# Performance work log

Hardware: AMD Instinct MI355X
Metric: run time of the kernel (lower is better)

## Reference

```python
import jax, jax.numpy as jnp
import numpy as np

B, T, N, R, I = 32, 512, 1024, 4, 8
DT = 0.1
G = 0.9


def setup_inputs() -> dict:
    key = jax.random.key(0)
    k1, k2, k3, k4, k5 = jax.random.split(key, 5)
    inputs = jax.random.normal(k1, (B, T, I, 1), dtype=jnp.float32)
    f = jax.random.normal(k2, (B, T, R, 1), dtype=jnp.float32)
    J = jax.random.normal(k3, (B, N, N), dtype=jnp.float32) * (G / np.sqrt(N))
    wIn = jax.random.normal(k4, (B, N, I), dtype=jnp.float32)
    m = jax.random.normal(k5, (B, N, R), dtype=jnp.float32)
    return {"inputs": inputs, "f": f, "J": J, "wIn": wIn, "m": m}


def _run(inputs, f, J, wIn, m):
    dt = DT
    dtype = inputs.dtype
    x0 = jnp.zeros((B, N, 1), dtype)
    n0 = jnp.zeros((B, N, R), dtype)
    P0 = jnp.tile(jnp.eye(N, dtype=dtype)[None] / 10.0, (B, 1, 1))

    def step(carry, t_in):
        x, P, n = carry
        u, f_t = t_in                               # u: (B,I,1), f_t: (B,R,1)
        # recurrence (r, z computed from PRE-update x, matching original)
        r = jnp.tanh(x)                             # (B,N,1)
        z = jnp.einsum('bnk,bns->bks', n, r)        # n^T @ r -> (B,R,1)
        x_new = (1.0 - dt) * x + dt * (J @ r + m @ z + wIn @ u)
        # RLS update (uses r from pre-update x)
        Pr = P @ r                                  # (B,N,1)
        rPr = jnp.sum(r * Pr, axis=1, keepdims=True)  # r^T P r -> (B,1,1)
        c = 1.0 / (1.0 + rPr)                       # scalar per batch
        P_new = P - c * (Pr @ jnp.swapaxes(Pr, -1, -2))
        err = z - f_t                               # (B,R,1)
        n_new = n - c * (Pr @ jnp.swapaxes(err, -1, -2))
        return (x_new, P_new, n_new), (x_new, z)

    u_seq = jnp.swapaxes(inputs, 0, 1)              # (T,B,I,1)
    f_seq = jnp.swapaxes(f, 0, 1)                   # (T,B,R,1)
    _, (xs, zs) = jax.lax.scan(step, (x0, P0, n0), (u_seq, f_seq))
    all_x = jnp.swapaxes(xs, 0, 1)                  # (B,T,N,1)
    all_z = jnp.swapaxes(zs, 0, 1)                  # (B,T,R,1)
    return all_x, all_z


def reference(inputs, f, J, wIn, m):
    return _run(inputs, f, J, wIn, m)
```

## Files before the change

### kernel.cpp

```cpp
#include <hip/hip_runtime.h>
#include <hip/hip_bf16.h>

#define BB 32
#define TT 512
#define NN 1024
#define RR 4
#define II 8
#define DT_C 0.1f

#define BPB 32
#define GRID (BB * BPB)

#define NBLK 32
#define ROWS (NN / NBLK)
#define VBLK 16

typedef __attribute__((ext_vector_type(8))) unsigned short ushort8v;

__device__ __forceinline__ float bf2f(unsigned short u) {
    union { unsigned int ui; float f; } cv; cv.ui = ((unsigned int)u) << 16; return cv.f;
}
__device__ __forceinline__ float bf2f_lo(unsigned int u) {
    union { unsigned int ui; float f; } cv; cv.ui = u << 16; return cv.f;
}
__device__ __forceinline__ float bf2f_hi(unsigned int u) {
    union { unsigned int ui; float f; } cv; cv.ui = u & 0xffff0000u; return cv.f;
}
__device__ __forceinline__ unsigned short f2bf_rne(float x) {
    union { float f; unsigned int ui; } cv; cv.f = x;
    unsigned int u = cv.ui; u += 0x7FFFu + ((u >> 16) & 1u);
    return (unsigned short)(u >> 16);
}
__device__ __forceinline__ float wave_reduce(float v) {
    #pragma unroll
    for (int off = 32; off; off >>= 1) v += __shfl_down(v, off, 64);
    return v;
}

__device__ __forceinline__ float llc_ldf(const float* p) {
    float r;
    asm volatile("global_load_dword %0, %1, off sc0 sc1\n\ts_waitcnt vmcnt(0)"
                 : "=&v"(r) : "v"(p) : "memory");
    return r;
}
__device__ __forceinline__ void llc_stf(float* p, float v) {
    asm volatile("global_store_dword %0, %1, off sc0 sc1" :: "v"(p), "v"(v) : "memory");
}
__device__ __forceinline__ void llc_st8(float* p, float a, float b) {
    float2 v; v.x = a; v.y = b;
    asm volatile("global_store_dwordx2 %0, %1, off sc0 sc1" :: "v"(p), "v"(v) : "memory");
}

__global__ __launch_bounds__(256) void k_convJl(const float* __restrict__ J,
                                                unsigned int* __restrict__ Jl) {
    const int b = blockIdx.x >> 5, k = blockIdx.x & 31;
    const int w = threadIdx.x >> 6, l = threadIdx.x & 63;
    unsigned int* dst = Jl + ((((size_t)(b * 32 + k) * 4 + w) * 64 + l) * 64);
    #pragma unroll
    for (int j = 0; j < 8; ++j) {
        const int row = k * 32 + w * 8 + j;
        const float* __restrict__ Jrow = J + ((size_t)b * NN + row) * NN;
        unsigned int out[8];
        #pragma unroll
        for (int e2 = 0; e2 < 8; ++e2) {
            const int c0 = l + 128 * e2;
            out[e2] = (unsigned int)f2bf_rne(Jrow[c0]) |
                      ((unsigned int)f2bf_rne(Jrow[c0 + 64]) << 16);
        }
        *(uint4*)(dst + j * 8)     = make_uint4(out[0], out[1], out[2], out[3]);
        *(uint4*)(dst + j * 8 + 4) = make_uint4(out[4], out[5], out[6], out[7]);
    }
}

__device__ __forceinline__ void batch_barrier(unsigned* cnt, unsigned* gen,
                                              unsigned expect) {
    asm volatile("s_waitcnt vmcnt(0) lgkmcnt(0)" ::: "memory");
    __syncthreads();
    if (threadIdx.x == 0) {
        unsigned old = __hip_atomic_fetch_add(cnt, 1u, __ATOMIC_RELAXED,
                                              __HIP_MEMORY_SCOPE_AGENT);
        if (old == BPB - 1u) {
            __hip_atomic_store(cnt, 0u, __ATOMIC_RELAXED, __HIP_MEMORY_SCOPE_AGENT);
            asm volatile("s_waitcnt vmcnt(0)" ::: "memory");
            __hip_atomic_fetch_add(gen, 1u, __ATOMIC_RELAXED, __HIP_MEMORY_SCOPE_AGENT);
        } else {
            while (__hip_atomic_load(gen, __ATOMIC_RELAXED, __HIP_MEMORY_SCOPE_AGENT)
                   < expect)
                __builtin_amdgcn_s_sleep(8);
        }
    }
    __syncthreads();
}

__global__ __launch_bounds__(256, 4) void k_persist(
    const unsigned int* __restrict__ Jl,
    float* __restrict__ rbuf,
    float* __restrict__ abuf,
    float* __restrict__ pa,
    float* __restrict__ sqpart,
    float* __restrict__ zr,
    unsigned* __restrict__ cnt, unsigned* __restrict__ gen,
    const float* __restrict__ m, const float* __restrict__ wIn,
    const float* __restrict__ inputs, const float* __restrict__ f,
    float* __restrict__ outx, float* __restrict__ outz)
{
    const int bid = blockIdx.x;
    const int b = (bid & 7) * 4 + (bid >> 8);
    const int k = (bid >> 3) & 31;
    const int tid = threadIdx.x, lane = tid & 63, wave = tid >> 6;
    const int row_loc = tid >> 3, sub = tid & 7;
    const int i_loc = k * 32 + row_loc;

    __shared__ unsigned short V_lds[32][512];
    __shared__ float r_sh[NN];
    __shared__ float a_sh[2 * TT / 2 + 512];
    __shared__ float sq32[32];
    __shared__ float r_next[32];
    __shared__ float Jr_sh[32];
    __shared__ float zred[32][4];
    __shared__ float zr2[128];
    __shared__ float red_sg[4];
    __shared__ float fsh[RR], ush[II], csh[2], zsh[RR], esh[RR];

    unsigned* mycnt = cnt + b * 32;
    unsigned* mygen = gen + b * 32;
    unsigned bar = 0;

    unsigned int jreg[64];
    {
        const uint4* jp = (const uint4*)(Jl +
            ((((size_t)(b * 32 + k) * 4 + wave) * 64 + lane) * 64));
        #pragma unroll
        for (int q = 0; q < 16; ++q) {
            uint4 v = jp[q];
            jreg[q * 4] = v.x; jreg[q * 4 + 1] = v.y;
            jreg[q * 4 + 2] = v.z; jreg[q * 4 + 3] = v.w;
        }
    }
    {
        unsigned long long* vz = (unsigned long long*)&V_lds[0][0];
        for (int q = tid; q < 32 * 512 / 4; q += 256) vz[q] = 0ull;
    }
    float4 nrow = {0.f, 0.f, 0.f, 0.f};
    float xreg = 0.f;
    if (sub == 0) llc_stf(rbuf + b * NN + i_loc, 0.f);
    if (tid < 4)  llc_stf(zr + b * 128 + k * 4 + tid, 0.f);
    batch_barrier(mycnt, mygen, ++bar);

    for (int t = 0; t < TT; ++t) {
        float4 rqf; float2 paw; float zrw;
        {
            const float* rp  = rbuf + b * NN + tid * 4;
            const float* pap = pa + ((size_t)b * 32 + (tid >> 3)) * TT
                                  + k * 16 + (tid & 7) * 2;
            const float* zp  = zr + b * 128 + (tid & 127);
            asm volatile(
                "global_load_dwordx4 %0, %3, off sc0 sc1\n\t"
                "global_load_dwordx2 %1, %4, off sc0 sc1\n\t"
                "global_load_dword   %2, %5, off sc0 sc1\n\t"
                "s_waitcnt vmcnt(0)"
                : "=&v"(rqf), "=&v"(paw), "=&v"(zrw)
                : "v"(rp), "v"(pap), "v"(zp)
                : "memory");
        }
        *(float4*)&r_sh[tid * 4] = rqf;
        zr2[tid & 127] = zrw;
        {
            const int s0g = k * 16 + (tid & 7) * 2;
            a_sh[tid]       = (s0g     < t) ? paw.x : 0.f;
            a_sh[256 + tid] = (s0g + 1 < t) ? paw.y : 0.f;
        }
        if (tid >= 136 && tid < 140) fsh[tid - 136] = f[((size_t)b * TT + t) * RR + (tid - 136)];
        if (tid >= 144 && tid < 152) ush[tid - 144] = inputs[((size_t)b * TT + t) * II + (tid - 144)];
        __syncthreads();
        if (tid < 8) {
            float A = 0.f, B = 0.f;
            #pragma unroll
            for (int kk = 0; kk < 32; ++kk) {
                A += a_sh[kk * 8 + tid];
                B += a_sh[256 + kk * 8 + tid];
            }
            llc_st8(abuf + b * TT + k * 16 + 2 * tid, A, B);
            float sq = A * A + B * B;
            sq += __shfl_down(sq, 4, 8);
            sq += __shfl_down(sq, 2, 8);
            sq += __shfl_down(sq, 1, 8);
            if (tid == 0) llc_stf(sqpart + b * 32 + k, sq);
        }
        batch_barrier(mycnt, mygen, ++bar);

        {
            float2 apw;
            const float* ap = abuf + b * TT + tid * 2;
            asm volatile("global_load_dwordx2 %0, %1, off sc0 sc1\n\ts_waitcnt vmcnt(0)"
                         : "=&v"(apw) : "v"(ap) : "memory");
            a_sh[2 * tid]     = apw.x;
            a_sh[2 * tid + 1] = apw.y;
        }
        {
            float sqr = 0.1f * (rqf.x * rqf.x + rqf.y * rqf.y +
                                rqf.z * rqf.z + rqf.w * rqf.w);
            sqr = wave_reduce(sqr);
            if (lane == 0) red_sg[wave] = sqr;
        }
        if (wave == 0 && lane < 32) sq32[lane] = llc_ldf(sqpart + b * 32 + lane);
        __syncthreads();

        float accJ[8] = {0.f, 0.f, 0.f, 0.f, 0.f, 0.f, 0.f, 0.f};
        #pragma unroll
        for (int e2 = 0; e2 < 8; ++e2) {
            const float rv0 = r_sh[lane + 128 * e2];
            const float rv1 = r_sh[lane + 128 * e2 + 64];
            #pragma unroll
            for (int j = 0; j < 8; ++j) {
                const unsigned int w = jreg[j * 8 + e2];
                accJ[j] = fmaf(bf2f_lo(w), rv0, accJ[j]);
                accJ[j] = fmaf(bf2f_hi(w), rv1, accJ[j]);
            }
        }
        #pragma unroll
        for (int j = 0; j < 8; ++j) {
            float v = wave_reduce(accJ[j]);
            if (lane == 0) Jr_sh[wave * 8 + j] = v;
        }

        if (tid == 0) {
            float sg = red_sg[0] + red_sg[1] + red_sg[2] + red_sg[3];
            float sa = 0.f;
            #pragma unroll
            for (int q = 0; q < 32; ++q) sa += sq32[q];
            const float c = 1.f / (1.f + (sg - sa));
            csh[0] = c; csh[1] = sqrtf(c);
        }
        if (tid < 4) {
            float zq = 0.f;
            #pragma unroll
            for (int kk = 0; kk < 32; ++kk) zq += zr2[kk * 4 + tid];
            zsh[tid] = zq;
            esh[tid] = zq - fsh[tid];
        }
        __syncthreads();

        float accp = 0.f;
        for (int mm = 0; mm * 64 < t; ++mm) {
            const int s0 = mm * 64 + sub * 8;
            const ushort8v vv = *(const ushort8v*)&V_lds[row_loc][s0];
            const float4 a0 = *(const float4*)&a_sh[s0];
            const float4 a1 = *(const float4*)&a_sh[s0 + 4];
            accp = fmaf(bf2f(vv[0]), a0.x, accp);
            accp = fmaf(bf2f(vv[1]), a0.y, accp);
            accp = fmaf(bf2f(vv[2]), a0.z, accp);
            accp = fmaf(bf2f(vv[3]), a0.w, accp);
            accp = fmaf(bf2f(vv[4]), a1.x, accp);
            accp = fmaf(bf2f(vv[5]), a1.y, accp);
            accp = fmaf(bf2f(vv[6]), a1.z, accp);
            accp = fmaf(bf2f(vv[7]), a1.w, accp);
        }
        accp += __shfl_down(accp, 4, 8);
        accp += __shfl_down(accp, 2, 8);
        accp += __shfl_down(accp, 1, 8);

        if (sub == 0) {
            const float c = csh[0], sqc = csh[1];
            const float pr = 0.1f * r_sh[i_loc] - accp;
            V_lds[row_loc][t] = f2bf_rne(sqc * pr);

            float accx = Jr_sh[row_loc];
            const float4 mv = *(const float4*)(m + ((size_t)b * NN + i_loc) * RR);
            accx = fmaf(mv.x, zsh[0], accx); accx = fmaf(mv.y, zsh[1], accx);
            accx = fmaf(mv.z, zsh[2], accx); accx = fmaf(mv.w, zsh[3], accx);
            const float4* __restrict__ wp =
                (const float4*)(wIn + ((size_t)b * NN + i_loc) * II);
            const float4 w0 = wp[0], w1 = wp[1];
            accx = fmaf(w0.x, ush[0], accx); accx = fmaf(w0.y, ush[1], accx);
            accx = fmaf(w0.z, ush[2], accx); accx = fmaf(w0.w, ush[3], accx);
            accx = fmaf(w1.x, ush[4], accx); accx = fmaf(w1.y, ush[5], accx);
            accx = fmaf(w1.z, ush[6], accx); accx = fmaf(w1.w, ush[7], accx);
            const float xn = (1.0f - DT_C) * xreg + DT_C * accx;
            xreg = xn;
            outx[((size_t)b * TT + t) * NN + i_loc] = xn;

            const float cpr = c * pr;
            nrow.x = fmaf(-cpr, esh[0], nrow.x);
            nrow.y = fmaf(-cpr, esh[1], nrow.y);
            nrow.z = fmaf(-cpr, esh[2], nrow.z);
            nrow.w = fmaf(-cpr, esh[3], nrow.w);

            const float rp2 = tanhf(xn);
            r_next[row_loc] = rp2;
            llc_stf(rbuf + b * NN + i_loc, rp2);
            ((float4*)zred)[row_loc] = make_float4(nrow.x * rp2, nrow.y * rp2,
                                                   nrow.z * rp2, nrow.w * rp2);
        }
        __syncthreads();

        if (t < TT - 1 && 2 * tid <= t) {
            const int s0 = 2 * tid;
            float A0 = 0.f, A1 = 0.f;
            #pragma unroll 8
            for (int i = 0; i < 32; ++i) {
                const unsigned vv = *(const unsigned*)&V_lds[i][s0];
                const float rv = r_next[i];
                A0 = fmaf(bf2f_lo(vv), rv, A0);
                A1 = fmaf(bf2f_hi(vv), rv, A1);
            }
            llc_st8(pa + ((size_t)b * 32 + k) * TT + s0, A0, A1);
        }
        if (tid < 4) {
            float zp = 0.f;
            #pragma unroll
            for (int i = 0; i < 32; ++i) zp += zred[i][tid];
            llc_stf(zr + b * 128 + k * 4 + tid, zp);
            if (k == 0) outz[((size_t)b * TT + t) * RR + tid] = zsh[tid];
        }
        batch_barrier(mycnt, mygen, ++bar);
    }
}

__global__ __launch_bounds__(256) void k_convJ_old(const float* __restrict__ J,
                                                   unsigned short* __restrict__ Jp) {
    const int row = blockIdx.x;
    const int tid = threadIdx.x;
    __shared__ float rowsh[NN];
    const float4* __restrict__ src = (const float4*)(J + (size_t)row * NN);
    float4* dst4 = (float4*)rowsh;
    for (int k = tid; k < NN / 4; k += 256) dst4[k] = src[k];
    __syncthreads();
    const int o0 = tid * 4;
    unsigned short out[4];
    #pragma unroll
    for (int j = 0; j < 4; ++j) {
        const int o = o0 + j;
        const int l = (o >> 3) & 63, g = o >> 9, e = o & 7;
        out[j] = f2bf_rne(rowsh[l + 64 * (8 * g + e)]);
    }
    uint2 w;
    w.x = (unsigned int)out[0] | ((unsigned int)out[1] << 16);
    w.y = (unsigned int)out[2] | ((unsigned int)out[3] << 16);
    *(uint2*)(Jp + (size_t)row * NN + o0) = w;
}

__global__ __launch_bounds__(256) void kA_fb(
    const float* __restrict__ x, const unsigned short* __restrict__ Jp,
    const unsigned short* __restrict__ Vp, const float* __restrict__ nmat,
    float* __restrict__ r_out, float* __restrict__ a_out,
    float* __restrict__ Jr, float* __restrict__ zbuf,
    float* __restrict__ part, int t)
{
    const int b   = blockIdx.x / (NBLK + VBLK);
    const int blk = blockIdx.x % (NBLK + VBLK);
    const int tid = threadIdx.x, lane = tid & 63, wave = tid >> 6;

    __shared__ float r_sh[NN];
    __shared__ float red_sh[4];

    for (int j = tid; j < NN; j += 256) {
        const float rv = tanhf(x[b * NN + j]);
        r_sh[j] = rv;
        if (blk == 0) r_out[b * NN + j] = rv;
    }
    __syncthreads();

    if (blk < NBLK) {
        for (int rr = wave; rr < ROWS; rr += 4) {
            const int row = blk * ROWS + rr;
            const ushort8v* __restrict__ Jrow =
                (const ushort8v*)(Jp + ((size_t)b * NN + row) * NN);
            const ushort8v jv0 = Jrow[lane];
            const ushort8v jv1 = Jrow[64 + lane];
            float acc = 0.0f;
            #pragma unroll
            for (int e = 0; e < 8; ++e) acc = fmaf(bf2f(jv0[e]), r_sh[lane + 64 * e], acc);
            #pragma unroll
            for (int e = 0; e < 8; ++e) acc = fmaf(bf2f(jv1[e]), r_sh[lane + 512 + 64 * e], acc);
            acc = wave_reduce(acc);
            if (lane == 0) Jr[b * NN + row] = acc;
        }
        if (blk == 0) {
            float p = 0.0f;
            for (int j = tid; j < NN; j += 256) p = fmaf(r_sh[j], r_sh[j], p);
            p = wave_reduce(p);
            if (lane == 0) red_sh[wave] = p;
            __syncthreads();
            if (tid == 0)
                part[b * 72 + 64] = 0.1f * (red_sh[0] + red_sh[1] + red_sh[2] + red_sh[3]);
            if (wave < RR) {
                float acc = 0.0f;
                for (int i2 = lane; i2 < NN; i2 += 64)
                    acc = fmaf(nmat[((size_t)b * NN + i2) * RR + wave], r_sh[i2], acc);
                acc = wave_reduce(acc);
                if (lane == 0) zbuf[b * RR + wave] = acc;
            }
        }
    } else {
        const int wid = (blk - NBLK) * 4 + wave;
        float negsum = 0.0f;
        for (int s = wid; s < t; s += 64) {
            const ushort8v* __restrict__ col =
                (const ushort8v*)(Vp + ((size_t)b * TT + s) * NN);
            const ushort8v vv0 = col[lane];
            const ushort8v vv1 = col[64 + lane];
            float acc = 0.0f;
            #pragma unroll
            for (int e = 0; e < 8; ++e) acc = fmaf(bf2f(vv0[e]), r_sh[lane + 64 * e], acc);
            #pragma unroll
            for (int e = 0; e < 8; ++e) acc = fmaf(bf2f(vv1[e]), r_sh[lane + 512 + 64 * e], acc);
            acc = wave_reduce(acc);
            if (lane == 0) {
                a_out[b * TT + s] = acc;
                negsum = fmaf(-acc, acc, negsum);
            }
        }
        if (lane == 0) part[b * 72 + wid] = negsum;
    }
}

__global__ __launch_bounds__(256) void kB_fb(
    unsigned short* __restrict__ Vp, const float* __restrict__ r,
    const float* __restrict__ a, const float* __restrict__ Jr,
    const float* __restrict__ zbuf, const float* __restrict__ part,
    float* __restrict__ x, float* __restrict__ nmat,
    const float* __restrict__ m, const float* __restrict__ wIn,
    const float* __restrict__ inputs, const float* __restrict__ f,
    float* __restrict__ outx, float* __restrict__ outz, int t)
{
    const int b   = blockIdx.x >> 3;
    const int tb  = blockIdx.x & 7;
    const int tid = threadIdx.x;
    const int pl    = tid & 63;
    const int slice = tid >> 6;

    __shared__ float a_sh[TT];
    __shared__ float ps[4][128];
    __shared__ float zsh[RR], esh[RR], ush[II];

    for (int s = tid; s < t; s += 256) a_sh[s] = a[b * TT + s];
    if (tid < RR) {
        const float zv = zbuf[b * RR + tid];
        zsh[tid] = zv;
        esh[tid] = zv - f[((size_t)b * TT + t) * RR + tid];
    }
    if (tid >= 64 && tid < 64 + II)
        ush[tid - 64] = inputs[((size_t)b * TT + t) * II + (tid - 64)];
    __syncthreads();

    const int p0 = (tb * 64 + pl) * 2;
    const unsigned short* __restrict__ Vb = Vp + (size_t)b * TT * NN;

    const int s_begin = (t * slice) >> 2;
    const int s_end   = (t * (slice + 1)) >> 2;
    float acc0 = 0.0f, acc1 = 0.0f;
    #pragma unroll 4
    for (int s = s_begin; s < s_end; ++s) {
        const unsigned int w = *(const unsigned int*)(Vb + (size_t)s * NN + p0);
        const float av = a_sh[s];
        acc0 = fmaf(bf2f((unsigned short)(w & 0xFFFFu)), av, acc0);
        acc1 = fmaf(bf2f((unsigned short)(w >> 16)), av, acc1);
    }
    ps[slice][pl * 2]     = acc0;
    ps[slice][pl * 2 + 1] = acc1;
    __syncthreads();

    if (slice == 0) {
        const int l = (p0 >> 3) & 63, g = p0 >> 9, e = p0 & 7;
        const int i0 = l + 64 * (8 * g + e);
        const int i1 = i0 + 64;
        const float s0 = ps[0][pl * 2] + ps[1][pl * 2] + ps[2][pl * 2] + ps[3][pl * 2];
        const float s1 = ps[0][pl * 2 + 1] + ps[1][pl * 2 + 1] + ps[2][pl * 2 + 1] + ps[3][pl * 2 + 1];

        float sg = 0.0f;
        #pragma unroll
        for (int q = 0; q < 65; ++q) sg += part[b * 72 + q];
        const float c  = 1.0f / (1.0f + sg);
        const float sq = sqrtf(c);

        const float pr0 = 0.1f * r[b * NN + i0] - s0;
        const float pr1 = 0.1f * r[b * NN + i1] - s1;

        unsigned int wv = (unsigned int)f2bf_rne(sq * pr0) |
                          ((unsigned int)f2bf_rne(sq * pr1) << 16);
        *(unsigned int*)(Vp + ((size_t)b * TT + t) * NN + p0) = wv;

        #pragma unroll
        for (int which = 0; which < 2; ++which) {
            const int   i  = which ? i1 : i0;
            const float pr = which ? pr1 : pr0;
            float acc = Jr[b * NN + i];
            const float4 mv = *(const float4*)(m + ((size_t)b * NN + i) * RR);
            acc = fmaf(mv.x, zsh[0], acc); acc = fmaf(mv.y, zsh[1], acc);
            acc = fmaf(mv.z, zsh[2], acc); acc = fmaf(mv.w, zsh[3], acc);
            const float4* __restrict__ wp = (const float4*)(wIn + ((size_t)b * NN + i) * II);
            const float4 w0 = wp[0], w1 = wp[1];
            acc = fmaf(w0.x, ush[0], acc); acc = fmaf(w0.y, ush[1], acc);
            acc = fmaf(w0.z, ush[2], acc); acc = fmaf(w0.w, ush[3], acc);
            acc = fmaf(w1.x, ush[4], acc); acc = fmaf(w1.y, ush[5], acc);
            acc = fmaf(w1.z, ush[6], acc); acc = fmaf(w1.w, ush[7], acc);
            const float xo = x[b * NN + i];
            const float xn = (1.0f - DT_C) * xo + DT_C * acc;
            x[b * NN + i] = xn;
            outx[((size_t)b * TT + t) * NN + i] = xn;

            float4* __restrict__ np = (float4*)(nmat + ((size_t)b * NN + i) * RR);
            float4 nv = *np;
            const float cpr = c * pr;
            nv.x = fmaf(-cpr, esh[0], nv.x); nv.y = fmaf(-cpr, esh[1], nv.y);
            nv.z = fmaf(-cpr, esh[2], nv.z); nv.w = fmaf(-cpr, esh[3], nv.w);
            *np = nv;
        }
    }
    if (tb == 0 && tid < RR) outz[((size_t)b * TT + t) * RR + tid] = zsh[tid];
}

extern "C" void kernel_launch(void* const* d_in, const int* in_sizes, int n_in,
                              void* d_out, int out_size, void* d_ws, size_t ws_size,
                              hipStream_t stream) {
    const float* inputs = (const float*)d_in[0];
    const float* f      = (const float*)d_in[1];
    const float* J      = (const float*)d_in[2];
    const float* wIn    = (const float*)d_in[3];
    const float* m      = (const float*)d_in[4];

    float* outx = (float*)d_out;
    float* outz = outx + (size_t)BB * TT * NN;

    char* ws = (char*)d_ws;
    size_t off = 0;
    unsigned int* Jl = (unsigned int*)(ws + off);  off += (size_t)BB * NN * NN * 2;
    unsigned short* Jp_fb = (unsigned short*)Jl;
    unsigned short* V1_fb = (unsigned short*)(ws + off); off += (size_t)BB * TT * NN * 2;
    float* pa     = (float*)(ws + off); off += (size_t)BB * 32 * TT * 4;
    float* rbuf   = (float*)(ws + off); off += (size_t)BB * NN * 4;
    float* abuf   = (float*)(ws + off); off += (size_t)BB * TT * 4;
    float* sqpart = (float*)(ws + off); off += (size_t)BB * 32 * 4;
    float* zrp    = (float*)(ws + off); off += (size_t)BB * 128 * 4;
    unsigned* cnt = (unsigned*)(ws + off); off += (size_t)BB * 32 * 4;
    unsigned* gen = (unsigned*)(ws + off); off += (size_t)BB * 32 * 4;
    float* x_fb   = (float*)(ws + off); off += (size_t)BB * NN * 4;
    float* nm     = (float*)(ws + off); off += (size_t)BB * NN * RR * 4;
    float* Jrb    = (float*)(ws + off); off += (size_t)BB * NN * 4;
    float* zb     = (float*)(ws + off); off += (size_t)BB * RR * 4 + 256;
    float* part72 = (float*)(ws + off); off += (size_t)BB * 72 * 4;

    hipMemsetAsync(cnt, 0, (size_t)BB * 32 * sizeof(unsigned), stream);
    hipMemsetAsync(gen, 0, (size_t)BB * 32 * sizeof(unsigned), stream);
    hipMemsetAsync(x_fb, 0, (size_t)BB * NN * sizeof(float), stream);
    hipMemsetAsync(nm,  0, (size_t)BB * NN * RR * sizeof(float), stream);

    k_convJl<<<BB * 32, 256, 0, stream>>>(J, Jl);

    void* kargs[] = {
        (void*)&Jl, (void*)&rbuf, (void*)&abuf, (void*)&pa,
        (void*)&sqpart, (void*)&zrp,
        (void*)&cnt, (void*)&gen,
        (void*)&m, (void*)&wIn, (void*)&inputs, (void*)&f,
        (void*)&outx, (void*)&outz
    };
    hipError_t rc = hipLaunchCooperativeKernel((const void*)k_persist,
                                               dim3(GRID), dim3(256),
                                               kargs, 0, stream);
    if (rc != hipSuccess) {
        k_convJ_old<<<BB * NN, 256, 0, stream>>>(J, Jp_fb);
        for (int t = 0; t < TT; ++t) {
            kA_fb<<<BB * (NBLK + VBLK), 256, 0, stream>>>(x_fb, Jp_fb, V1_fb, nm,
                                                          rbuf, abuf, Jrb, zb, part72, t);
            kB_fb<<<BB * 8, 256, 0, stream>>>(V1_fb, rbuf, abuf, Jrb, zb, part72,
                                              x_fb, nm, m, wIn, inputs, f, outx, outz, t);
        }
    }
}
```

Before: 9.476 ms.

## Replace per-block partial buffers with atomic accumulation to drop one grid barrier per step

Each step now accumulates the a-vector and z partials directly with device-scope float atomics into a triple-buffered global slot, instead of writing per-block partials, barrier-syncing, and reducing them. This removes one batch-wide barrier and a round of global loads per timestep, and folds the a·a term into the local reduction for c. The V_lds row pitch is padded to 516 to reduce LDS bank conflicts, and the loads are adjusted to fit the new alignment. In exchange it adds atomic contention and makes the summation order nondeterministic. It also needs the future slot to be zeroed ahead of use.

```diff
diff --git a/kernel.cpp b/kernel.cpp
--- a/kernel.cpp
+++ b/kernel.cpp
@@ -15,6 +15,8 @@
 #define ROWS (NN / NBLK)
 #define VBLK 16
 
+#define VPITCH 516
+
 typedef __attribute__((ext_vector_type(8))) unsigned short ushort8v;
 
 __device__ __forceinline__ float bf2f(unsigned short u) {
@@ -37,12 +39,6 @@
     return v;
 }
 
-__device__ __forceinline__ float llc_ldf(const float* p) {
-    float r;
-    asm volatile("global_load_dword %0, %1, off sc0 sc1\n\ts_waitcnt vmcnt(0)"
-                 : "=&v"(r) : "v"(p) : "memory");
-    return r;
-}
 __device__ __forceinline__ void llc_stf(float* p, float v) {
     asm volatile("global_store_dword %0, %1, off sc0 sc1" :: "v"(p), "v"(v) : "memory");
 }
@@ -95,10 +91,8 @@
 __global__ __launch_bounds__(256, 4) void k_persist(
     const unsigned int* __restrict__ Jl,
     float* __restrict__ rbuf,
-    float* __restrict__ abuf,
-    float* __restrict__ pa,
-    float* __restrict__ sqpart,
-    float* __restrict__ zr,
+    float* __restrict__ aalt,
+    float* __restrict__ zslot,
     unsigned* __restrict__ cnt, unsigned* __restrict__ gen,
     const float* __restrict__ m, const float* __restrict__ wIn,
     const float* __restrict__ inputs, const float* __restrict__ f,
@@ -111,14 +105,12 @@
     const int row_loc = tid >> 3, sub = tid & 7;
     const int i_loc = k * 32 + row_loc;
 
-    __shared__ unsigned short V_lds[32][512];
+    __shared__ unsigned short V_lds[32][VPITCH];
     __shared__ float r_sh[NN];
-    __shared__ float a_sh[2 * TT / 2 + 512];
-    __shared__ float sq32[32];
+    __shared__ float a_sh[TT];
+    __shared__ float zred[32][4];
     __shared__ float r_next[32];
     __shared__ float Jr_sh[32];
-    __shared__ float zred[32][4];
-    __shared__ float zr2[128];
     __shared__ float red_sg[4];
     __shared__ float fsh[RR], ush[II], csh[2], zsh[RR], esh[RR];
 
@@ -138,73 +130,67 @@
         }
     }
     {
-        unsigned long long* vz = (unsigned long long*)&V_lds[0][0];
-        for (int q = tid; q < 32 * 512 / 4; q += 256) vz[q] = 0ull;
+        unsigned int* vz = (unsigned int*)&V_lds[0][0];
+        for (int q = tid; q < 32 * VPITCH / 2; q += 256) vz[q] = 0u;
     }
     float4 nrow = {0.f, 0.f, 0.f, 0.f};
     float xreg = 0.f;
     if (sub == 0) llc_stf(rbuf + b * NN + i_loc, 0.f);
-    if (tid < 4)  llc_stf(zr + b * 128 + k * 4 + tid, 0.f);
+    if (tid < 8) {
+        llc_st8(aalt + ((size_t)b * 3 + 0) * 512 + k * 16 + 2 * tid, 0.f, 0.f);
+        llc_st8(aalt + ((size_t)b * 3 + 1) * 512 + k * 16 + 2 * tid, 0.f, 0.f);
+    }
+    if (k == 0 && tid < 16) llc_stf(zslot + b * 24 + tid, 0.f);
     batch_barrier(mycnt, mygen, ++bar);
 
+    int cur = 0;
     for (int t = 0; t < TT; ++t) {
-        float4 rqf; float2 paw; float zrw;
+        const int nxt = (cur == 2) ? 0 : cur + 1;
+        const int fut = (nxt == 2) ? 0 : nxt + 1;
+        float* acur = aalt + ((size_t)b * 3 + cur) * 512;
+        float* anxt = aalt + ((size_t)b * 3 + nxt) * 512;
+        float* afut = aalt + ((size_t)b * 3 + fut) * 512;
+        float* zcur = zslot + (b * 3 + cur) * 8;
+        float* znxt = zslot + (b * 3 + nxt) * 8;
+        float* zfut = zslot + (b * 3 + fut) * 8;
+
+        float4 rqf; float2 aw; float zw;
         {
-            const float* rp  = rbuf + b * NN + tid * 4;
-            const float* pap = pa + ((size_t)b * 32 + (tid >> 3)) * TT
-                                  + k * 16 + (tid & 7) * 2;
-            const float* zp  = zr + b * 128 + (tid & 127);
+            const float* rp = rbuf + b * NN + tid * 4;
+            const float* ap = acur + tid * 2;
+            const float* zp = (tid < 4) ? (zcur + tid) : rp;
             asm volatile(
                 "global_load_dwordx4 %0, %3, off sc0 sc1\n\t"
                 "global_load_dwordx2 %1, %4, off sc0 sc1\n\t"
                 "global_load_dword   %2, %5, off sc0 sc1\n\t"
                 "s_waitcnt vmcnt(0)"
-                : "=&v"(rqf), "=&v"(paw), "=&v"(zrw)
-                : "v"(rp), "v"(pap), "v"(zp)
+                : "=&v"(rqf), "=&v"(aw), "=&v"(zw)
+                : "v"(rp), "v"(ap), "v"(zp)
                 : "memory");
         }
         *(float4*)&r_sh[tid * 4] = rqf;
-        zr2[tid & 127] = zrw;
-        {
-            const int s0g = k * 16 + (tid & 7) * 2;
-            a_sh[tid]       = (s0g     < t) ? paw.x : 0.f;
-            a_sh[256 + tid] = (s0g + 1 < t) ? paw.y : 0.f;
-        }
+        *(float2*)&a_sh[tid * 2] = aw;
         if (tid >= 136 && tid < 140) fsh[tid - 136] = f[((size_t)b * TT + t) * RR + (tid - 136)];
         if (tid >= 144 && tid < 152) ush[tid - 144] = inputs[((size_t)b * TT + t) * II + (tid - 144)];
+        {
+            float sloc = 0.1f * (rqf.x * rqf.x + rqf.y * rqf.y +
+                                 rqf.z * rqf.z + rqf.w * rqf.w)
+                         - (aw.x * aw.x + aw.y * aw.y);
+            sloc = wave_reduce(sloc);
+            if (lane == 0) red_sg[wave] = sloc;
+        }
         __syncthreads();
-        if (tid < 8) {
-            float A = 0.f, B = 0.f;
-            #pragma unroll
-            for (int kk = 0; kk < 32; ++kk) {
-                A += a_sh[kk * 8 + tid];
-                B += a_sh[256 + kk * 8 + tid];
-            }
-            llc_st8(abuf + b * TT + k * 16 + 2 * tid, A, B);
-            float sq = A * A + B * B;
-            sq += __shfl_down(sq, 4, 8);
-            sq += __shfl_down(sq, 2, 8);
-            sq += __shfl_down(sq, 1, 8);
-            if (tid == 0) llc_stf(sqpart + b * 32 + k, sq);
-        }
-        batch_barrier(mycnt, mygen, ++bar);
-
-        {
-            float2 apw;
-            const float* ap = abuf + b * TT + tid * 2;
-            asm volatile("global_load_dwordx2 %0, %1, off sc0 sc1\n\ts_waitcnt vmcnt(0)"
-                         : "=&v"(apw) : "v"(ap) : "memory");
-            a_sh[2 * tid]     = apw.x;
-            a_sh[2 * tid + 1] = apw.y;
-        }
-        {
-            float sqr = 0.1f * (rqf.x * rqf.x + rqf.y * rqf.y +
-                                rqf.z * rqf.z + rqf.w * rqf.w);
-            sqr = wave_reduce(sqr);
-            if (lane == 0) red_sg[wave] = sqr;
-        }
-        if (wave == 0 && lane < 32) sq32[lane] = llc_ldf(sqpart + b * 32 + lane);
-        __syncthreads();
+
+        if (tid == 0) {
+            const float sg = red_sg[0] + red_sg[1] + red_sg[2] + red_sg[3];
+            const float c = 1.f / (1.f + sg);
+            csh[0] = c; csh[1] = sqrtf(c);
+        }
+        if (tid < 4) {
+            zsh[tid] = zw;
+            esh[tid] = zw - fsh[tid];
+            if (k == 0) outz[((size_t)b * TT + t) * RR + tid] = zw;
+        }
 
         float accJ[8] = {0.f, 0.f, 0.f, 0.f, 0.f, 0.f, 0.f, 0.f};
         #pragma unroll
@@ -224,41 +210,26 @@
             if (lane == 0) Jr_sh[wave * 8 + j] = v;
         }
 
-        if (tid == 0) {
-            float sg = red_sg[0] + red_sg[1] + red_sg[2] + red_sg[3];
-            float sa = 0.f;
-            #pragma unroll
-            for (int q = 0; q < 32; ++q) sa += sq32[q];
-            const float c = 1.f / (1.f + (sg - sa));
-            csh[0] = c; csh[1] = sqrtf(c);
-        }
-        if (tid < 4) {
-            float zq = 0.f;
-            #pragma unroll
-            for (int kk = 0; kk < 32; ++kk) zq += zr2[kk * 4 + tid];
-            zsh[tid] = zq;
-            esh[tid] = zq - fsh[tid];
-        }
-        __syncthreads();
-
         float accp = 0.f;
         for (int mm = 0; mm * 64 < t; ++mm) {
-            const int s0 = mm * 64 + sub * 8;
-            const ushort8v vv = *(const ushort8v*)&V_lds[row_loc][s0];
-            const float4 a0 = *(const float4*)&a_sh[s0];
-            const float4 a1 = *(const float4*)&a_sh[s0 + 4];
-            accp = fmaf(bf2f(vv[0]), a0.x, accp);
-            accp = fmaf(bf2f(vv[1]), a0.y, accp);
-            accp = fmaf(bf2f(vv[2]), a0.z, accp);
-            accp = fmaf(bf2f(vv[3]), a0.w, accp);
-            accp = fmaf(bf2f(vv[4]), a1.x, accp);
-            accp = fmaf(bf2f(vv[5]), a1.y, accp);
-            accp = fmaf(bf2f(vv[6]), a1.z, accp);
-            accp = fmaf(bf2f(vv[7]), a1.w, accp);
+            const int c8 = (mm * 8 + sub) * 8;
+            const uint2 v01 = *(const uint2*)&V_lds[row_loc][c8];
+            const uint2 v23 = *(const uint2*)&V_lds[row_loc][c8 + 4];
+            const float4 a0 = *(const float4*)&a_sh[c8];
+            const float4 a1 = *(const float4*)&a_sh[c8 + 4];
+            accp = fmaf(bf2f_lo(v01.x), a0.x, accp);
+            accp = fmaf(bf2f_hi(v01.x), a0.y, accp);
+            accp = fmaf(bf2f_lo(v01.y), a0.z, accp);
+            accp = fmaf(bf2f_hi(v01.y), a0.w, accp);
+            accp = fmaf(bf2f_lo(v23.x), a1.x, accp);
+            accp = fmaf(bf2f_hi(v23.x), a1.y, accp);
+            accp = fmaf(bf2f_lo(v23.y), a1.z, accp);
+            accp = fmaf(bf2f_hi(v23.y), a1.w, accp);
         }
         accp += __shfl_down(accp, 4, 8);
         accp += __shfl_down(accp, 2, 8);
         accp += __shfl_down(accp, 1, 8);
+        __syncthreads();
 
         if (sub == 0) {
             const float c = csh[0], sqc = csh[1];
@@ -294,26 +265,35 @@
         }
         __syncthreads();
 
-        if (t < TT - 1 && 2 * tid <= t) {
+        if (t < TT - 1) {
             const int s0 = 2 * tid;
-            float A0 = 0.f, A1 = 0.f;
-            #pragma unroll 8
-            for (int i = 0; i < 32; ++i) {
-                const unsigned vv = *(const unsigned*)&V_lds[i][s0];
-                const float rv = r_next[i];
-                A0 = fmaf(bf2f_lo(vv), rv, A0);
-                A1 = fmaf(bf2f_hi(vv), rv, A1);
+            if (s0 <= t) {
+                float A0 = 0.f, A1 = 0.f;
+                #pragma unroll 8
+                for (int i = 0; i < 32; ++i) {
+                    const unsigned vv = *(const unsigned*)&V_lds[i][s0];
+                    const float rv = r_next[i];
+                    A0 = fmaf(bf2f_lo(vv), rv, A0);
+                    A1 = fmaf(bf2f_hi(vv), rv, A1);
+                }
+                __hip_atomic_fetch_add(anxt + s0, A0, __ATOMIC_RELAXED,
+                                       __HIP_MEMORY_SCOPE_AGENT);
+                __hip_atomic_fetch_add(anxt + s0 + 1, A1, __ATOMIC_RELAXED,
+                                       __HIP_MEMORY_SCOPE_AGENT);
             }
-            llc_st8(pa + ((size_t)b * 32 + k) * TT + s0, A0, A1);
-        }
-        if (tid < 4) {
-            float zp = 0.f;
-            #pragma unroll
-            for (int i = 0; i < 32; ++i) zp += zred[i][tid];
-            llc_stf(zr + b * 128 + k * 4 + tid, zp);
-            if (k == 0) outz[((size_t)b * TT + t) * RR + tid] = zsh[tid];
-        }
+            if (tid < 4) {
+                float zp = 0.f;
+                #pragma unroll
+                for (int i = 0; i < 32; ++i) zp += zred[i][tid];
+                __hip_atomic_fetch_add(znxt + tid, zp, __ATOMIC_RELAXED,
+                                       __HIP_MEMORY_SCOPE_AGENT);
+            }
+        }
+        if (tid < 8) llc_st8(afut + k * 16 + 2 * tid, 0.f, 0.f);
+        if (k == 0 && tid < 4) llc_stf(zfut + tid, 0.f);
+
         batch_barrier(mycnt, mygen, ++bar);
+        cur = nxt;
     }
 }
 
@@ -528,15 +508,15 @@
     unsigned int* Jl = (unsigned int*)(ws + off);  off += (size_t)BB * NN * NN * 2;
     unsigned short* Jp_fb = (unsigned short*)Jl;
     unsigned short* V1_fb = (unsigned short*)(ws + off); off += (size_t)BB * TT * NN * 2;
-    float* pa     = (float*)(ws + off); off += (size_t)BB * 32 * TT * 4;
     float* rbuf   = (float*)(ws + off); off += (size_t)BB * NN * 4;
-    float* abuf   = (float*)(ws + off); off += (size_t)BB * TT * 4;
-    float* sqpart = (float*)(ws + off); off += (size_t)BB * 32 * 4;
-    float* zrp    = (float*)(ws + off); off += (size_t)BB * 128 * 4;
+    float* aalt   = (float*)(ws + off); off += (size_t)BB * 3 * 512 * 4;
+    float* zslot  = (float*)(ws + off); off += (size_t)BB * 3 * 8 * 4;
     unsigned* cnt = (unsigned*)(ws + off); off += (size_t)BB * 32 * 4;
     unsigned* gen = (unsigned*)(ws + off); off += (size_t)BB * 32 * 4;
     float* x_fb   = (float*)(ws + off); off += (size_t)BB * NN * 4;
     float* nm     = (float*)(ws + off); off += (size_t)BB * NN * RR * 4;
+    float* abuf   = (float*)(ws + off); off += (size_t)BB * TT * 4;
+    float* rfb    = (float*)(ws + off); off += (size_t)BB * NN * 4;
     float* Jrb    = (float*)(ws + off); off += (size_t)BB * NN * 4;
     float* zb     = (float*)(ws + off); off += (size_t)BB * RR * 4 + 256;
     float* part72 = (float*)(ws + off); off += (size_t)BB * 72 * 4;
@@ -549,8 +529,7 @@
     k_convJl<<<BB * 32, 256, 0, stream>>>(J, Jl);
 
     void* kargs[] = {
-        (void*)&Jl, (void*)&rbuf, (void*)&abuf, (void*)&pa,
-        (void*)&sqpart, (void*)&zrp,
+        (void*)&Jl, (void*)&rbuf, (void*)&aalt, (void*)&zslot,
         (void*)&cnt, (void*)&gen,
         (void*)&m, (void*)&wIn, (void*)&inputs, (void*)&f,
         (void*)&outx, (void*)&outz
@@ -562,8 +541,8 @@
         k_convJ_old<<<BB * NN, 256, 0, stream>>>(J, Jp_fb);
         for (int t = 0; t < TT; ++t) {
             kA_fb<<<BB * (NBLK + VBLK), 256, 0, stream>>>(x_fb, Jp_fb, V1_fb, nm,
-                                                          rbuf, abuf, Jrb, zb, part72, t);
-            kB_fb<<<BB * 8, 256, 0, stream>>>(V1_fb, rbuf, abuf, Jrb, zb, part72,
+                                                          rfb, abuf, Jrb, zb, part72, t);
+            kB_fb<<<BB * 8, 256, 0, stream>>>(V1_fb, rfb, abuf, Jrb, zb, part72,
                                               x_fb, nm, m, wIn, inputs, f, outx, outz, t);
         }
     }
```

Result: slower. 12.80 ms (+35.1%).
